# Kernel optimization log

Measured on AMD Instinct MI355X. Metric: run time of the kernel, lower is better.

The kernel has to match this reference:

```python
import jax, jax.numpy as jnp
import numpy as np

N_NODES = 100000
N_EDGES = 1600000
NFEAT = 256
NHID = 128
NCLASS = 8


def setup_inputs() -> dict:
    key = jax.random.key(0)
    k1, k2, k3, k4, k5 = jax.random.split(key, 5)
    x = jax.random.normal(k1, (N_NODES, NFEAT), dtype=jnp.float32)
    edge_index = jax.random.randint(k2, (2, N_EDGES), 0, N_NODES, dtype=jnp.int64)
    # GCNConv weight (glorot) and bias
    s1 = float(np.sqrt(6.0 / (NFEAT + NHID)))
    W1 = jax.random.uniform(k3, (NFEAT, NHID), dtype=jnp.float32, minval=-s1, maxval=s1)
    b1 = jnp.zeros((NHID,), dtype=jnp.float32)
    # fc Linear (xavier uniform per weights_init, bias zero)
    s2 = float(np.sqrt(6.0 / (NHID + NCLASS)))
    Wfc = jax.random.uniform(k4, (NHID, NCLASS), dtype=jnp.float32, minval=-s2, maxval=s2)
    bfc = jnp.zeros((NCLASS,), dtype=jnp.float32)
    return {"x": x, "edge_index": edge_index, "W1": W1, "b1": b1, "Wfc": Wfc, "bfc": bfc}


def gcn_conv(x, src, dst, W, b, n_nodes):
    # PyG GCNConv: h = X W; out_i = sum_j norm_ij * h_j over A+I with sym norm
    h = x @ W  # [N, nhid]
    deg = jax.ops.segment_sum(jnp.ones_like(dst, dtype=h.dtype), dst, num_segments=n_nodes)
    dinv = jnp.where(deg > 0, jax.lax.rsqrt(deg), 0.0)  # deg^{-1/2}
    norm = dinv[src] * dinv[dst]  # [E+N]
    msg = h[src] * norm[:, None]  # gather + scale, [E+N, nhid]
    out = jax.ops.segment_sum(msg, dst, num_segments=n_nodes)
    return out + b


def reference(x, edge_index, W1, b1, Wfc, bfc):
    n = x.shape[0]
    loop = jnp.arange(n, dtype=edge_index.dtype)
    src = jnp.concatenate([edge_index[0], loop])  # add self-loops
    dst = jnp.concatenate([edge_index[1], loop])
    h = gcn_conv(x, src, dst, W1, b1, n)  # GCN_Body (no activation in forward)
    return h @ Wfc + bfc  # fc
```

## Files before the change

### kernel.cpp

```cpp
#include <hip/hip_runtime.h>

#define N_NODES 100000
#define NFEAT 256
#define NHID 128
#define NCLASS 8

#define BSH 8
#define BUCK 256
#define NBUCK ((N_NODES + BUCK - 1) / BUCK)
#define VX 8
#define CAPS 704
#define GSTRIDE (NBUCK * CAPS)
#define CAPB (CAPS * VX)
#define NBLK1 2048
#define ZBLKS ((N_NODES + 255) / 256)
#define OVF_CAP 32768

__global__ __launch_bounds__(512) void init_kernel(const float* __restrict__ W1,
        const float* __restrict__ b1, const float* __restrict__ Wfc,
        const float* __restrict__ bfc, float* __restrict__ Wf,
        float* __restrict__ cvec, int* __restrict__ gcur, int* __restrict__ ovf_cnt) {
    int tid = threadIdx.x;
    if (blockIdx.x == 0) {
        __shared__ float wfs[NHID * NCLASS];
        __shared__ float bs[NHID];
        for (int i = tid; i < NHID * NCLASS; i += 512) wfs[i] = Wfc[i];
        if (tid < NHID) bs[tid] = b1[tid];
        __syncthreads();
        if (tid < NFEAT) {
            float acc[NCLASS] = {};
            for (int h = 0; h < NHID; h++) {
                float w = W1[tid * NHID + h];
                #pragma unroll
                for (int c = 0; c < NCLASS; c++) acc[c] += w * wfs[h * NCLASS + c];
            }
            #pragma unroll
            for (int c = 0; c < NCLASS; c++) Wf[tid * NCLASS + c] = acc[c];
        }
        if (tid < NCLASS) {
            float a = bfc[tid];
            for (int h = 0; h < NHID; h++) a += bs[h] * wfs[h * NCLASS + tid];
            cvec[tid] = a;
        }
    } else {
        int i = (blockIdx.x - 1) * 512 + tid;
        if (i < VX * NBUCK) {
            int g = i / NBUCK;
            int b = i - g * NBUCK;
            gcur[i] = g * GSTRIDE + b * CAPS;
        }
        if (blockIdx.x == 1 && tid == 0) *ovf_cnt = 0;
    }
}

__global__ __launch_bounds__(256) void scat_z_kernel(const int* __restrict__ esrc,
        const int* __restrict__ edst, int* __restrict__ gcur,
        int* __restrict__ ebufP, int* __restrict__ ovf_cnt,
        int* __restrict__ ovfbuf,
        const float* __restrict__ X, const float* __restrict__ Wf,
        float* __restrict__ Zs, int chunk, int nE, int n) {
    __shared__ int h[NBUCK];
    __shared__ int lcur[NBUCK];
    int tid = threadIdx.x;

    if (blockIdx.x < ZBLKS) {
        int row = blockIdx.x * 256 + tid;
        bool ok = row < n;
        int r = ok ? row : n - 1;
        const float4* xr = (const float4*)(X + (long)r * NFEAT);
        float acc[NCLASS] = {};
        #pragma unroll 8
        for (int k = 0; k < 64; k++) {
            float4 x4 = xr[k];
            const float* w = Wf + k * 32;
            #pragma unroll
            for (int c = 0; c < NCLASS; c++)
                acc[c] += x4.x * w[c] + x4.y * w[8 + c]
                        + x4.z * w[16 + c] + x4.w * w[24 + c];
        }
        if (ok) {
            float4 o0, o1;
            o0.x = acc[0]; o0.y = acc[1]; o0.z = acc[2]; o0.w = acc[3];
            o1.x = acc[4]; o1.y = acc[5]; o1.z = acc[6]; o1.w = acc[7];
            ((float4*)Zs)[(long)row * 2]     = o0;
            ((float4*)Zs)[(long)row * 2 + 1] = o1;
        }
    } else {
        int bid = blockIdx.x - ZBLKS;
        int xcc;
        asm volatile("s_getreg_b32 %0, hwreg(HW_REG_XCC_ID)" : "=s"(xcc));
        xcc &= (VX - 1);
        for (int i = tid; i < NBUCK; i += 256) h[i] = 0;
        __syncthreads();
        int e0 = bid * chunk;
        int e1 = min(e0 + chunk, nE);
        for (int e = e0 + tid * 4; e + 3 < e1; e += 1024) {
            int4 d = *(const int4*)&edst[e];
            atomicAdd(&h[d.x >> BSH], 1); atomicAdd(&h[d.y >> BSH], 1);
            atomicAdd(&h[d.z >> BSH], 1); atomicAdd(&h[d.w >> BSH], 1);
        }
        int full = e0 + ((e1 - e0) & ~3);
        if (full + tid < e1) atomicAdd(&h[edst[full + tid] >> BSH], 1);
        __syncthreads();
        const int gbase = xcc * GSTRIDE;
        for (int b = tid; b < NBUCK; b += 256) {
            int c = h[b];
            lcur[b] = c ? atomicAdd(&gcur[xcc * NBUCK + b], c) : 0;
        }
        __syncthreads();
        for (int e = e0 + tid * 4; e + 3 < e1; e += 1024) {
            int4 s = *(const int4*)&esrc[e];
            int4 d = *(const int4*)&edst[e];
            int b0 = d.x >> BSH, b1_ = d.y >> BSH, b2 = d.z >> BSH, b3 = d.w >> BSH;
            int p0 = atomicAdd(&lcur[b0], 1);
            int p1 = atomicAdd(&lcur[b1_], 1);
            int p2 = atomicAdd(&lcur[b2], 1);
            int p3 = atomicAdd(&lcur[b3], 1);
            int k0 = (s.x << BSH) | (d.x & (BUCK - 1));
            int k1 = (s.y << BSH) | (d.y & (BUCK - 1));
            int k2 = (s.z << BSH) | (d.z & (BUCK - 1));
            int k3 = (s.w << BSH) | (d.w & (BUCK - 1));
            if (p0 < gbase + b0 * CAPS + CAPS) ebufP[p0] = k0;
            else { int op = atomicAdd(ovf_cnt, 1); if (op < OVF_CAP) { ovfbuf[2*op] = k0; ovfbuf[2*op+1] = b0; } }
            if (p1 < gbase + b1_ * CAPS + CAPS) ebufP[p1] = k1;
            else { int op = atomicAdd(ovf_cnt, 1); if (op < OVF_CAP) { ovfbuf[2*op] = k1; ovfbuf[2*op+1] = b1_; } }
            if (p2 < gbase + b2 * CAPS + CAPS) ebufP[p2] = k2;
            else { int op = atomicAdd(ovf_cnt, 1); if (op < OVF_CAP) { ovfbuf[2*op] = k2; ovfbuf[2*op+1] = b2; } }
            if (p3 < gbase + b3 * CAPS + CAPS) ebufP[p3] = k3;
            else { int op = atomicAdd(ovf_cnt, 1); if (op < OVF_CAP) { ovfbuf[2*op] = k3; ovfbuf[2*op+1] = b3; } }
        }
        if (full + tid < e1) {
            int s = esrc[full + tid], d = edst[full + tid];
            int b = d >> BSH;
            int p = atomicAdd(&lcur[b], 1);
            int k = (s << BSH) | (d & (BUCK - 1));
            if (p < gbase + b * CAPS + CAPS) ebufP[p] = k;
            else { int op = atomicAdd(ovf_cnt, 1); if (op < OVF_CAP) { ovfbuf[2*op] = k; ovfbuf[2*op+1] = b; } }
        }
    }
}

__global__ __launch_bounds__(512) void deg_dinv_kernel(const int* __restrict__ ebufP,
        const int* __restrict__ gcur, const int* __restrict__ ovf_cnt,
        const int* __restrict__ ovfbuf, float* __restrict__ dinv) {
    __shared__ int cnt[BUCK];
    int b = blockIdx.x, tid = threadIdx.x;
    if (tid < BUCK) cnt[tid] = 0;
    __syncthreads();
    #pragma unroll
    for (int g = 0; g < VX; g++) {
        int base = g * GSTRIDE + b * CAPS;
        int end = min(gcur[g * NBUCK + b], base + CAPS);
        int n = end - base;
        const int4* p4 = (const int4*)&ebufP[base];
        int n4 = n >> 2;
        for (int k = tid; k < n4; k += 512) {
            int4 p = p4[k];
            atomicAdd(&cnt[p.x & (BUCK - 1)], 1);
            atomicAdd(&cnt[p.y & (BUCK - 1)], 1);
            atomicAdd(&cnt[p.z & (BUCK - 1)], 1);
            atomicAdd(&cnt[p.w & (BUCK - 1)], 1);
        }
        for (int k = (n4 << 2) + tid; k < n; k += 512)
            atomicAdd(&cnt[ebufP[base + k] & (BUCK - 1)], 1);
    }
    int nov = min(*ovf_cnt, OVF_CAP);
    for (int i = tid; i < nov; i += 512)
        if (ovfbuf[2 * i + 1] == b) atomicAdd(&cnt[ovfbuf[2 * i] & (BUCK - 1)], 1);
    __syncthreads();
    if (tid < BUCK) {
        int node = (b << BSH) + tid;
        if (node < N_NODES) dinv[node] = rsqrtf((float)(cnt[tid] + 1));
    }
}

__global__ __launch_bounds__(512) void sort_gather_kernel(
        const float* __restrict__ Zs,
        const int* __restrict__ ebufP,
        const int* __restrict__ gcur,
        const int* __restrict__ ovf_cnt,
        const int* __restrict__ ovfbuf,
        const float* __restrict__ dinv,
        const float* __restrict__ cvec,
        float* __restrict__ out, int n) {
    __shared__ int cnt[BUCK];
    __shared__ int off[BUCK + 1];
    __shared__ int ss[BUCK];
    __shared__ int sorted[CAPB];
    int b = blockIdx.x, tid = threadIdx.x;
    const float4* Zs4 = (const float4*)Zs;
    float4 c0v = ((const float4*)cvec)[0];
    float4 c1v = ((const float4*)cvec)[1];
    int nov = min(*ovf_cnt, OVF_CAP);

    if (tid < BUCK) cnt[tid] = 0;
    __syncthreads();
    #pragma unroll
    for (int g = 0; g < VX; g++) {
        int base = g * GSTRIDE + b * CAPS;
        int end = min(gcur[g * NBUCK + b], base + CAPS);
        int nn = end - base;
        const int4* p4 = (const int4*)&ebufP[base];
        int n4 = nn >> 2;
        for (int k = tid; k < n4; k += 512) {
            int4 p = p4[k];
            atomicAdd(&cnt[p.x & (BUCK - 1)], 1);
            atomicAdd(&cnt[p.y & (BUCK - 1)], 1);
            atomicAdd(&cnt[p.z & (BUCK - 1)], 1);
            atomicAdd(&cnt[p.w & (BUCK - 1)], 1);
        }
        for (int k = (n4 << 2) + tid; k < nn; k += 512)
            atomicAdd(&cnt[ebufP[base + k] & (BUCK - 1)], 1);
    }
    for (int i = tid; i < nov; i += 512)
        if (ovfbuf[2 * i + 1] == b) atomicAdd(&cnt[ovfbuf[2 * i] & (BUCK - 1)], 1);
    __syncthreads();

    int t = (tid < BUCK) ? cnt[tid] : 0;
    if (tid < BUCK) ss[tid] = t;
    __syncthreads();
    for (int o = 1; o < BUCK; o <<= 1) {
        int u = 0;
        if (tid < BUCK && tid >= o) u = ss[tid - o];
        __syncthreads();
        if (tid < BUCK) ss[tid] += u;
        __syncthreads();
    }
    if (tid < BUCK) {
        off[tid] = ss[tid] - t;
        cnt[tid] = ss[tid] - t;
        if (tid == BUCK - 1) off[BUCK] = ss[tid];
    }
    __syncthreads();

    #pragma unroll
    for (int g = 0; g < VX; g++) {
        int base = g * GSTRIDE + b * CAPS;
        int end = min(gcur[g * NBUCK + b], base + CAPS);
        int nn = end - base;
        const int4* p4 = (const int4*)&ebufP[base];
        int n4 = nn >> 2;
        for (int k = tid; k < n4; k += 512) {
            int4 p = p4[k];
            int s0 = atomicAdd(&cnt[p.x & (BUCK - 1)], 1);
            int s1 = atomicAdd(&cnt[p.y & (BUCK - 1)], 1);
            int s2 = atomicAdd(&cnt[p.z & (BUCK - 1)], 1);
            int s3 = atomicAdd(&cnt[p.w & (BUCK - 1)], 1);
            sorted[s0] = p.x >> BSH;
            sorted[s1] = p.y >> BSH;
            sorted[s2] = p.z >> BSH;
            sorted[s3] = p.w >> BSH;
        }
        for (int k = (n4 << 2) + tid; k < nn; k += 512) {
            int p = ebufP[base + k];
            int slot = atomicAdd(&cnt[p & (BUCK - 1)], 1);
            sorted[slot] = p >> BSH;
        }
    }
    for (int i = tid; i < nov; i += 512) {
        if (ovfbuf[2 * i + 1] == b) {
            int p = ovfbuf[2 * i];
            int slot = atomicAdd(&cnt[p & (BUCK - 1)], 1);
            sorted[slot] = p >> BSH;
        }
    }
    __syncthreads();

    int li = tid >> 1;
    int hh = tid & 1;
    int node = (b << BSH) + li;
    if (node < n) {
        int k0 = off[li], k1 = off[li + 1];
        float4 a; a.x = 0.f; a.y = 0.f; a.z = 0.f; a.w = 0.f;
        int k = k0;
        for (; k + 1 < k1; k += 2) {
            int s0 = sorted[k], s1 = sorted[k + 1];
            float dv0 = dinv[s0], dv1 = dinv[s1];
            float4 z0 = Zs4[s0 * 2 + hh];
            float4 z1 = Zs4[s1 * 2 + hh];
            a.x += dv0 * z0.x + dv1 * z1.x; a.y += dv0 * z0.y + dv1 * z1.y;
            a.z += dv0 * z0.z + dv1 * z1.z; a.w += dv0 * z0.w + dv1 * z1.w;
        }
        if (k < k1) {
            int s = sorted[k];
            float dv = dinv[s];
            float4 z = Zs4[s * 2 + hh];
            a.x += dv * z.x; a.y += dv * z.y; a.z += dv * z.z; a.w += dv * z.w;
        }
        float dd = rsqrtf((float)(k1 - k0 + 1));
        float4 zs = Zs4[node * 2 + hh];
        a.x += dd * zs.x; a.y += dd * zs.y;
        a.z += dd * zs.z; a.w += dd * zs.w;
        float4 cv = hh ? c1v : c0v;
        float4 o;
        o.x = a.x * dd + cv.x; o.y = a.y * dd + cv.y;
        o.z = a.z * dd + cv.z; o.w = a.w * dd + cv.w;
        ((float4*)out)[node * 2 + hh] = o;
    }
}

extern "C" void kernel_launch(void* const* d_in, const int* in_sizes, int n_in,
                              void* d_out, int out_size, void* d_ws, size_t ws_size,
                              hipStream_t stream) {
    const float* x    = (const float*)d_in[0];
    const int*   eidx = (const int*)d_in[1];
    const float* W1   = (const float*)d_in[2];
    const float* b1   = (const float*)d_in[3];
    const float* Wfc  = (const float*)d_in[4];
    const float* bfc  = (const float*)d_in[5];
    float* out = (float*)d_out;

    const int N = N_NODES;
    const int E = in_sizes[1] / 2;

    const int* esrc = eidx;
    const int* edst = eidx + E;

    float* Zs     = (float*)d_ws;
    float* cvec   = Zs + (long)8 * N;
    float* Wf     = cvec + 8;
    float* dinv   = Wf + NFEAT * NCLASS;
    int*   gcur   = (int*)(dinv + N);
    int*   ovfc   = gcur + VX * NBUCK;
    int*   ovfbuf = ovfc + 4;
    int*   ebufP  = ovfbuf + 2 * OVF_CAP;

    const int chunk = (((E + NBLK1 - 1) / NBLK1) + 3) & ~3;

    init_kernel<<<1 + (VX * NBUCK + 511) / 512, 512, 0, stream>>>(
        W1, b1, Wfc, bfc, Wf, cvec, gcur, ovfc);
    scat_z_kernel<<<ZBLKS + NBLK1, 256, 0, stream>>>(
        esrc, edst, gcur, ebufP, ovfc, ovfbuf, x, Wf, Zs, chunk, E, N);
    deg_dinv_kernel<<<NBUCK, 512, 0, stream>>>(ebufP, gcur, ovfc, ovfbuf, dinv);
    sort_gather_kernel<<<NBUCK, 512, 0, stream>>>(Zs, ebufP, gcur, ovfc, ovfbuf, dinv, cvec, out, N);
}
```

Before: 219.8 us.

## Fuse degree and sort-gather kernels with cooperative grid sync

Merges the separate degree/dinv kernel into the sort-gather kernel. Each block writes dinv for its own bucket from the histogram it already builds, then a grid-wide cooperative sync makes all dinv values visible before the gather phase. This removes a full second pass over the edge buckets and one kernel launch. In exchange it needs a cooperative launch with all 391 blocks of 512 threads and about 25 KB of shared memory resident at once, plus the cost of a grid barrier.

```diff
diff --git a/kernel.cpp b/kernel.cpp
--- a/kernel.cpp
+++ b/kernel.cpp
@@ -1,4 +1,7 @@
 #include <hip/hip_runtime.h>
+#include <hip/hip_cooperative_groups.h>
+
+namespace cg = cooperative_groups;
 
 #define N_NODES 100000
 #define NFEAT 256
@@ -140,48 +143,14 @@
     }
 }
 
-__global__ __launch_bounds__(512) void deg_dinv_kernel(const int* __restrict__ ebufP,
-        const int* __restrict__ gcur, const int* __restrict__ ovf_cnt,
-        const int* __restrict__ ovfbuf, float* __restrict__ dinv) {
-    __shared__ int cnt[BUCK];
-    int b = blockIdx.x, tid = threadIdx.x;
-    if (tid < BUCK) cnt[tid] = 0;
-    __syncthreads();
-    #pragma unroll
-    for (int g = 0; g < VX; g++) {
-        int base = g * GSTRIDE + b * CAPS;
-        int end = min(gcur[g * NBUCK + b], base + CAPS);
-        int n = end - base;
-        const int4* p4 = (const int4*)&ebufP[base];
-        int n4 = n >> 2;
-        for (int k = tid; k < n4; k += 512) {
-            int4 p = p4[k];
-            atomicAdd(&cnt[p.x & (BUCK - 1)], 1);
-            atomicAdd(&cnt[p.y & (BUCK - 1)], 1);
-            atomicAdd(&cnt[p.z & (BUCK - 1)], 1);
-            atomicAdd(&cnt[p.w & (BUCK - 1)], 1);
-        }
-        for (int k = (n4 << 2) + tid; k < n; k += 512)
-            atomicAdd(&cnt[ebufP[base + k] & (BUCK - 1)], 1);
-    }
-    int nov = min(*ovf_cnt, OVF_CAP);
-    for (int i = tid; i < nov; i += 512)
-        if (ovfbuf[2 * i + 1] == b) atomicAdd(&cnt[ovfbuf[2 * i] & (BUCK - 1)], 1);
-    __syncthreads();
-    if (tid < BUCK) {
-        int node = (b << BSH) + tid;
-        if (node < N_NODES) dinv[node] = rsqrtf((float)(cnt[tid] + 1));
-    }
-}
-
-__global__ __launch_bounds__(512) void sort_gather_kernel(
+__global__ __launch_bounds__(512) void deg_sort_gather_kernel(
         const float* __restrict__ Zs,
         const int* __restrict__ ebufP,
         const int* __restrict__ gcur,
         const int* __restrict__ ovf_cnt,
         const int* __restrict__ ovfbuf,
-        const float* __restrict__ dinv,
         const float* __restrict__ cvec,
+        float* __restrict__ dinv,
         float* __restrict__ out, int n) {
     __shared__ int cnt[BUCK];
     __shared__ int off[BUCK + 1];
@@ -217,7 +186,11 @@
     __syncthreads();
 
     int t = (tid < BUCK) ? cnt[tid] : 0;
-    if (tid < BUCK) ss[tid] = t;
+    if (tid < BUCK) {
+        int node = (b << BSH) + tid;
+        if (node < n) dinv[node] = rsqrtf((float)(t + 1));
+        ss[tid] = t;
+    }
     __syncthreads();
     for (int o = 1; o < BUCK; o <<= 1) {
         int u = 0;
@@ -264,7 +237,9 @@
             sorted[slot] = p >> BSH;
         }
     }
-    __syncthreads();
+
+    __threadfence();
+    cg::this_grid().sync();
 
     int li = tid >> 1;
     int hh = tid & 1;
@@ -331,6 +306,13 @@
         W1, b1, Wfc, bfc, Wf, cvec, gcur, ovfc);
     scat_z_kernel<<<ZBLKS + NBLK1, 256, 0, stream>>>(
         esrc, edst, gcur, ebufP, ovfc, ovfbuf, x, Wf, Zs, chunk, E, N);
-    deg_dinv_kernel<<<NBUCK, 512, 0, stream>>>(ebufP, gcur, ovfc, ovfbuf, dinv);
-    sort_gather_kernel<<<NBUCK, 512, 0, stream>>>(Zs, ebufP, gcur, ovfc, ovfbuf, dinv, cvec, out, N);
+
+    const float* ZsC = Zs; const int* ebufC = ebufP; const int* gcurC = gcur;
+    const int* ovfcC = ovfc; const int* ovfbC = ovfbuf; const float* cvecC = cvec;
+    float* dinvC = dinv; float* outC = out; int nC = N;
+    void* kargs[] = { (void*)&ZsC, (void*)&ebufC, (void*)&gcurC, (void*)&ovfcC,
+                      (void*)&ovfbC, (void*)&cvecC, (void*)&dinvC, (void*)&outC,
+                      (void*)&nC };
+    hipLaunchCooperativeKernel((const void*)deg_sort_gather_kernel,
+                               dim3(NBUCK), dim3(512), kargs, 0, stream);
 }
```

Result: slower. 322.1 us (+46.5%).
